# Optimization experiments

Measured on AMD Instinct MI355X. Metric: run time of the kernel, lower is better.

Reference implementation:

```python
import jax, jax.numpy as jnp
import numpy as np

B = 1048576
EPS = 1e-5

def _lin_params(key, din, dout):
    k1, k2 = jax.random.split(key)
    bound = 1.0 / np.sqrt(din)
    w = jax.random.uniform(k1, (din, dout), minval=-bound, maxval=bound, dtype=jnp.float32)
    b = jax.random.uniform(k2, (dout,), minval=-bound, maxval=bound, dtype=jnp.float32)
    return w, b

def setup_inputs() -> dict:
    key = jax.random.key(0)
    ks = jax.random.split(key, 10)
    x = jax.random.normal(ks[0], (B, 8), dtype=jnp.float32)
    dims = [(8, 16), (16, 16), (16, 12), (12, 8), (8, 4), (4, 4), (4, 4), (4, 1)]
    names = ['fm', 'c1', 'p1', 'c2', 'p2', 'c3', 'r', 'h']
    inp = {'x': x,
           'bn_g': jnp.ones((8,), jnp.float32),
           'bn_b': jnp.zeros((8,), jnp.float32)}
    for i, (nm, (di, do)) in enumerate(zip(names, dims)):
        w, b = _lin_params(ks[i + 1], di, do)
        inp['w_' + nm] = w
        inp['b_' + nm] = b
    return inp

def reference(x, bn_g, bn_b, w_fm, b_fm, w_c1, b_c1, w_p1, b_p1, w_c2, b_c2,
              w_p2, b_p2, w_c3, b_c3, w_r, b_r, w_h, b_h):
    # BatchNorm1d (training mode): batch statistics, biased variance
    mu = jnp.mean(x, axis=0)
    var = jnp.mean((x - mu) ** 2, axis=0)
    h = (x - mu) * jax.lax.rsqrt(var + EPS) * bn_g + bn_b
    h = jnp.tanh(h @ w_fm + b_fm)   # [B,16] feature_map
    h = jnp.tanh(h @ w_c1 + b_c1)   # [B,16] conv1
    h = jnp.tanh(h @ w_p1 + b_p1)   # [B,12] pool1
    h = jnp.tanh(h @ w_c2 + b_c2)   # [B,8]  conv2
    h = jnp.tanh(h @ w_p2 + b_p2)   # [B,4]  pool2
    h = jnp.tanh(h @ w_c3 + b_c3)   # [B,4]  conv3
    res = jax.nn.relu(h @ w_r + b_r)  # [B,4] residual branch
    h = h + res
    return jax.nn.sigmoid(h @ w_h + b_h)  # [B,1]
```

## Files before the change

kernel.cpp:

```cpp
#include <hip/hip_runtime.h>
#include <stdint.h>

#define B_ROWS 1048576
#define STAT_BLOCKS 512
#define MAIN_BLOCKS 2048

typedef __fp16 h2 __attribute__((ext_vector_type(2)));

#define PART_OFF 16
#define WPK_OFF 8208
#define BIA_OFF 8578
#define W_FM 0
#define W_C1 64
#define W_P1 192
#define W_C2 288
#define W_P2 336
#define W_C3 352
#define W_R  360
#define W_H  368
#define B_FM 0
#define B_C1 16
#define B_P1 32
#define B_C2 44
#define B_P2 52
#define B_C3 56
#define B_R  60
#define B_H  64

__device__ __forceinline__ float exp_tanh(float x) {
    float e = __builtin_amdgcn_exp2f(x * 2.8853900817779268f);
    return 1.0f - 2.0f * __builtin_amdgcn_rcpf(e + 1.0f);
}

__device__ __forceinline__ float fast_sigmoid(float x) {
    float e = __builtin_amdgcn_exp2f(x * -1.4426950408889634f);
    return __builtin_amdgcn_rcpf(1.0f + e);
}

template<int DIN, int DOUT>
__device__ void pack_layer(const float* __restrict__ w, const float* __restrict__ b,
                           uint32_t* __restrict__ wdst, float* __restrict__ bdst) {
    for (int idx = threadIdx.x; idx < DOUT * (DIN / 2); idx += blockDim.x) {
        int j = idx / (DIN / 2), i2 = idx % (DIN / 2);
        h2 h;
        h.x = (__fp16)w[(2 * i2) * DOUT + j];
        h.y = (__fp16)w[(2 * i2 + 1) * DOUT + j];
        wdst[j * (DIN / 2) + i2] = __builtin_bit_cast(uint32_t, h);
    }
    for (int j = threadIdx.x; j < DOUT; j += blockDim.x) bdst[j] = b[j];
}

__global__ __launch_bounds__(256) void bn_stats(
    const float* __restrict__ x, float* __restrict__ ws,
    const float* __restrict__ w_c1, const float* __restrict__ b_c1,
    const float* __restrict__ w_p1, const float* __restrict__ b_p1,
    const float* __restrict__ w_c2, const float* __restrict__ b_c2,
    const float* __restrict__ w_p2, const float* __restrict__ b_p2,
    const float* __restrict__ w_c3, const float* __restrict__ b_c3,
    const float* __restrict__ w_r,  const float* __restrict__ b_r,
    const float* __restrict__ w_h,  const float* __restrict__ b_h)
{
    const int tid = blockIdx.x * 256 + threadIdx.x;
    float s[8], q[8];
#pragma unroll
    for (int c = 0; c < 8; ++c) { s[c] = 0.f; q[c] = 0.f; }
    const float4* x4 = (const float4*)x;
#pragma unroll
    for (int k = 0; k < 8; ++k) {
        int r = tid + k * 131072;
        float4 a = x4[2 * r];
        float4 b = x4[2 * r + 1];
        s[0] += a.x; s[1] += a.y; s[2] += a.z; s[3] += a.w;
        s[4] += b.x; s[5] += b.y; s[6] += b.z; s[7] += b.w;
        q[0] += a.x * a.x; q[1] += a.y * a.y; q[2] += a.z * a.z; q[3] += a.w * a.w;
        q[4] += b.x * b.x; q[5] += b.y * b.y; q[6] += b.z * b.z; q[7] += b.w * b.w;
    }
#pragma unroll
    for (int off = 32; off > 0; off >>= 1) {
#pragma unroll
        for (int c = 0; c < 8; ++c) {
            s[c] += __shfl_down(s[c], off);
            q[c] += __shfl_down(q[c], off);
        }
    }
    __shared__ float red[4][16];
    const int lane = threadIdx.x & 63;
    const int wave = threadIdx.x >> 6;
    if (lane == 0) {
#pragma unroll
        for (int c = 0; c < 8; ++c) { red[wave][c] = s[c]; red[wave][8 + c] = q[c]; }
    }
    __syncthreads();
    if (threadIdx.x < 16) {
        float acc = red[0][threadIdx.x] + red[1][threadIdx.x] +
                    red[2][threadIdx.x] + red[3][threadIdx.x];
        ws[PART_OFF + blockIdx.x * 16 + threadIdx.x] = acc;
    }
    if (blockIdx.x == 0) {
        uint32_t* wpk = (uint32_t*)(ws + WPK_OFF);
        float*    bpk = ws + BIA_OFF;
        pack_layer<16,16>(w_c1, b_c1, wpk + W_C1, bpk + B_C1);
        pack_layer<16,12>(w_p1, b_p1, wpk + W_P1, bpk + B_P1);
        pack_layer<12, 8>(w_c2, b_c2, wpk + W_C2, bpk + B_C2);
        pack_layer<8,  4>(w_p2, b_p2, wpk + W_P2, bpk + B_P2);
        pack_layer<4,  4>(w_c3, b_c3, wpk + W_C3, bpk + B_C3);
        pack_layer<4,  4>(w_r,  b_r,  wpk + W_R,  bpk + B_R);
        pack_layer<4,  1>(w_h,  b_h,  wpk + W_H,  bpk + B_H);
    }
}

__global__ __launch_bounds__(256) void bn_finalize(
    const float* __restrict__ bn_g, const float* __restrict__ bn_b,
    const float* __restrict__ w_fm, const float* __restrict__ b_fm,
    float* __restrict__ ws)
{
    __shared__ float accs[16][17];
    __shared__ float scs[8], shs[8];
    const int f = threadIdx.x & 15;
    const int chunk = threadIdx.x >> 4;
    const float* p = ws + PART_OFF + (chunk * 32) * 16 + f;
    float a = 0.f;
#pragma unroll 8
    for (int b = 0; b < 32; ++b) a += p[b * 16];
    accs[chunk][f] = a;
    __syncthreads();
    if (threadIdx.x < 16) {
        float t = 0.f;
#pragma unroll
        for (int c = 0; c < 16; ++c) t += accs[c][threadIdx.x];
        accs[0][threadIdx.x] = t;
    }
    __syncthreads();
    if (threadIdx.x < 8) {
        const float invB = 1.0f / (float)B_ROWS;
        int c = threadIdx.x;
        float mu  = accs[0][c] * invB;
        float var = fmaf(-mu, mu, accs[0][8 + c] * invB);
        float sv  = bn_g[c] * rsqrtf(var + 1e-5f);
        scs[c] = sv;
        shs[c] = fmaf(-mu, sv, bn_b[c]);
    }
    __syncthreads();
    if (threadIdx.x < 64) {
        int j = threadIdx.x >> 2, i2 = threadIdx.x & 3;
        h2 h;
        h.x = (__fp16)(w_fm[(2 * i2) * 16 + j]     * scs[2 * i2]);
        h.y = (__fp16)(w_fm[(2 * i2 + 1) * 16 + j] * scs[2 * i2 + 1]);
        ((uint32_t*)(ws + WPK_OFF))[W_FM + j * 4 + i2] = __builtin_bit_cast(uint32_t, h);
    }
    if (threadIdx.x < 16) {
        int j = threadIdx.x;
        float acc = b_fm[j];
#pragma unroll
        for (int i = 0; i < 8; ++i) acc = fmaf(shs[i], w_fm[i * 16 + j], acc);
        (ws + BIA_OFF)[B_FM + j] = acc;
    }
}

template<int DIN, int DOUT>
__device__ __forceinline__ void layer_dot1(const h2* __restrict__ apk,
                                           float* __restrict__ o,
                                           const uint32_t* __restrict__ wpk,
                                           const float* __restrict__ bias) {
#pragma unroll
    for (int j = 0; j < DOUT; ++j) {
        float acc = bias[j];
#pragma unroll
        for (int i2 = 0; i2 < DIN / 2; ++i2) {
            h2 w = __builtin_bit_cast(h2, wpk[j * (DIN / 2) + i2]);
            acc = __builtin_amdgcn_fdot2(apk[i2], w, acc, false);
        }
        o[j] = acc;
    }
}

template<int N>
__device__ __forceinline__ void tanh_pack1(const float* __restrict__ in,
                                           h2* __restrict__ pk) {
#pragma unroll
    for (int k = 0; k < N / 2; ++k) {
        float t0 = exp_tanh(in[2 * k]);
        float t1 = exp_tanh(in[2 * k + 1]);
        pk[k] = __builtin_amdgcn_cvt_pkrtz(t0, t1);
    }
}

__device__ __forceinline__ float row_forward(float4 x0, float4 x1,
        const uint32_t* __restrict__ wpk, const float* __restrict__ bpk) {
    h2 a[4];
    a[0] = __builtin_amdgcn_cvt_pkrtz(x0.x, x0.y);
    a[1] = __builtin_amdgcn_cvt_pkrtz(x0.z, x0.w);
    a[2] = __builtin_amdgcn_cvt_pkrtz(x1.x, x1.y);
    a[3] = __builtin_amdgcn_cvt_pkrtz(x1.z, x1.w);

    float o1[16]; h2 p1[8];
    layer_dot1<8, 16>(a, o1, wpk + W_FM, bpk + B_FM);
    tanh_pack1<16>(o1, p1);
    float o2[16]; h2 p2[8];
    layer_dot1<16,16>(p1, o2, wpk + W_C1, bpk + B_C1);
    tanh_pack1<16>(o2, p2);
    float o3[12]; h2 p3[6];
    layer_dot1<16,12>(p2, o3, wpk + W_P1, bpk + B_P1);
    tanh_pack1<12>(o3, p3);
    float o4[8]; h2 p4[4];
    layer_dot1<12, 8>(p3, o4, wpk + W_C2, bpk + B_C2);
    tanh_pack1<8>(o4, p4);
    float o5[4]; h2 p5[2];
    layer_dot1<8,  4>(p4, o5, wpk + W_P2, bpk + B_P2);
    tanh_pack1<4>(o5, p5);
    float c4[4];
    layer_dot1<4,  4>(p5, c4, wpk + W_C3, bpk + B_C3);

    float f[4];
#pragma unroll
    for (int j = 0; j < 4; ++j) f[j] = exp_tanh(c4[j]);
    h2 pc[2];
    pc[0] = __builtin_amdgcn_cvt_pkrtz(f[0], f[1]);
    pc[1] = __builtin_amdgcn_cvt_pkrtz(f[2], f[3]);
    float r4[4];
    layer_dot1<4,  4>(pc, r4, wpk + W_R, bpk + B_R);
#pragma unroll
    for (int j = 0; j < 4; ++j) f[j] += fmaxf(r4[j], 0.f);
    h2 ph[2];
    ph[0] = __builtin_amdgcn_cvt_pkrtz(f[0], f[1]);
    ph[1] = __builtin_amdgcn_cvt_pkrtz(f[2], f[3]);
    float oh[1];
    layer_dot1<4,  1>(ph, oh, wpk + W_H, bpk + B_H);
    return fast_sigmoid(oh[0]);
}

__global__ __launch_bounds__(256, 6) void qcnn_main(
    const float* __restrict__ x, const float* __restrict__ ws,
    float* __restrict__ out)
{
    const int tid = blockIdx.x * 256 + threadIdx.x;
    const int r0 = tid, r1 = tid + (B_ROWS / 2);
    const float4* x4 = (const float4*)x;
    float4 xa0 = x4[2 * r0], xa1 = x4[2 * r0 + 1];
    float4 xb0 = x4[2 * r1], xb1 = x4[2 * r1 + 1];

    const uint32_t* wpk = (const uint32_t*)(ws + WPK_OFF);
    const float*    bpk = ws + BIA_OFF;

    out[r0] = row_forward(xa0, xa1, wpk, bpk);
    out[r1] = row_forward(xb0, xb1, wpk, bpk);
}

extern "C" void kernel_launch(void* const* d_in, const int* in_sizes, int n_in,
                              void* d_out, int out_size, void* d_ws, size_t ws_size,
                              hipStream_t stream) {
    const float* x    = (const float*)d_in[0];
    const float* bn_g = (const float*)d_in[1];
    const float* bn_b = (const float*)d_in[2];
    const float* w_fm = (const float*)d_in[3];
    const float* b_fm = (const float*)d_in[4];
    const float* w_c1 = (const float*)d_in[5];
    const float* b_c1 = (const float*)d_in[6];
    const float* w_p1 = (const float*)d_in[7];
    const float* b_p1 = (const float*)d_in[8];
    const float* w_c2 = (const float*)d_in[9];
    const float* b_c2 = (const float*)d_in[10];
    const float* w_p2 = (const float*)d_in[11];
    const float* b_p2 = (const float*)d_in[12];
    const float* w_c3 = (const float*)d_in[13];
    const float* b_c3 = (const float*)d_in[14];
    const float* w_r  = (const float*)d_in[15];
    const float* b_r  = (const float*)d_in[16];
    const float* w_h  = (const float*)d_in[17];
    const float* b_h  = (const float*)d_in[18];
    float* out = (float*)d_out;
    float* ws  = (float*)d_ws;

    bn_stats<<<STAT_BLOCKS, 256, 0, stream>>>(
        x, ws, w_c1, b_c1, w_p1, b_p1, w_c2, b_c2,
        w_p2, b_p2, w_c3, b_c3, w_r, b_r, w_h, b_h);
    bn_finalize<<<1, 256, 0, stream>>>(bn_g, bn_b, w_fm, b_fm, ws);
    qcnn_main<<<MAIN_BLOCKS, 256, 0, stream>>>(x, ws, out);
}
```

Baseline: 139.2 us.

## Fold BN finalize into main kernel and process four rows per thread

Removes the single-block bn_finalize launch. Each main-kernel block now redundantly reduces the 512 partial sums to BN scale and shift, and applies them per row with FMAs before fp16 packing, instead of folding them into the first-layer weights. The main grid is halved so each thread handles four rows as two adjacent pairs with float2 output stores. This trades one kernel launch and its serialization for redundant per-block reduction work, extra per-row normalization arithmetic, and block-level synchronization at kernel start.

```diff
diff --git a/kernel.cpp b/kernel.cpp
--- a/kernel.cpp
+++ b/kernel.cpp
@@ -3,7 +3,7 @@
 
 #define B_ROWS 1048576
 #define STAT_BLOCKS 512
-#define MAIN_BLOCKS 2048
+#define MAIN_BLOCKS 1024
 
 typedef __fp16 h2 __attribute__((ext_vector_type(2)));
 
@@ -52,6 +52,7 @@
 
 __global__ __launch_bounds__(256) void bn_stats(
     const float* __restrict__ x, float* __restrict__ ws,
+    const float* __restrict__ w_fm, const float* __restrict__ b_fm,
     const float* __restrict__ w_c1, const float* __restrict__ b_c1,
     const float* __restrict__ w_p1, const float* __restrict__ b_p1,
     const float* __restrict__ w_c2, const float* __restrict__ b_c2,
@@ -99,6 +100,7 @@
     if (blockIdx.x == 0) {
         uint32_t* wpk = (uint32_t*)(ws + WPK_OFF);
         float*    bpk = ws + BIA_OFF;
+        pack_layer<8, 16>(w_fm, b_fm, wpk + W_FM, bpk + B_FM);
         pack_layer<16,16>(w_c1, b_c1, wpk + W_C1, bpk + B_C1);
         pack_layer<16,12>(w_p1, b_p1, wpk + W_P1, bpk + B_P1);
         pack_layer<12, 8>(w_c2, b_c2, wpk + W_C2, bpk + B_C2);
@@ -109,54 +111,6 @@
     }
 }
 
-__global__ __launch_bounds__(256) void bn_finalize(
-    const float* __restrict__ bn_g, const float* __restrict__ bn_b,
-    const float* __restrict__ w_fm, const float* __restrict__ b_fm,
-    float* __restrict__ ws)
-{
-    __shared__ float accs[16][17];
-    __shared__ float scs[8], shs[8];
-    const int f = threadIdx.x & 15;
-    const int chunk = threadIdx.x >> 4;
-    const float* p = ws + PART_OFF + (chunk * 32) * 16 + f;
-    float a = 0.f;
-#pragma unroll 8
-    for (int b = 0; b < 32; ++b) a += p[b * 16];
-    accs[chunk][f] = a;
-    __syncthreads();
-    if (threadIdx.x < 16) {
-        float t = 0.f;
-#pragma unroll
-        for (int c = 0; c < 16; ++c) t += accs[c][threadIdx.x];
-        accs[0][threadIdx.x] = t;
-    }
-    __syncthreads();
-    if (threadIdx.x < 8) {
-        const float invB = 1.0f / (float)B_ROWS;
-        int c = threadIdx.x;
-        float mu  = accs[0][c] * invB;
-        float var = fmaf(-mu, mu, accs[0][8 + c] * invB);
-        float sv  = bn_g[c] * rsqrtf(var + 1e-5f);
-        scs[c] = sv;
-        shs[c] = fmaf(-mu, sv, bn_b[c]);
-    }
-    __syncthreads();
-    if (threadIdx.x < 64) {
-        int j = threadIdx.x >> 2, i2 = threadIdx.x & 3;
-        h2 h;
-        h.x = (__fp16)(w_fm[(2 * i2) * 16 + j]     * scs[2 * i2]);
-        h.y = (__fp16)(w_fm[(2 * i2 + 1) * 16 + j] * scs[2 * i2 + 1]);
-        ((uint32_t*)(ws + WPK_OFF))[W_FM + j * 4 + i2] = __builtin_bit_cast(uint32_t, h);
-    }
-    if (threadIdx.x < 16) {
-        int j = threadIdx.x;
-        float acc = b_fm[j];
-#pragma unroll
-        for (int i = 0; i < 8; ++i) acc = fmaf(shs[i], w_fm[i * 16 + j], acc);
-        (ws + BIA_OFF)[B_FM + j] = acc;
-    }
-}
-
 template<int DIN, int DOUT>
 __device__ __forceinline__ void layer_dot1(const h2* __restrict__ apk,
                                            float* __restrict__ o,
@@ -186,12 +140,17 @@
 }
 
 __device__ __forceinline__ float row_forward(float4 x0, float4 x1,
+        const float* __restrict__ sc, const float* __restrict__ sh,
         const uint32_t* __restrict__ wpk, const float* __restrict__ bpk) {
+    float n[8];
+    n[0] = fmaf(x0.x, sc[0], sh[0]); n[1] = fmaf(x0.y, sc[1], sh[1]);
+    n[2] = fmaf(x0.z, sc[2], sh[2]); n[3] = fmaf(x0.w, sc[3], sh[3]);
+    n[4] = fmaf(x1.x, sc[4], sh[4]); n[5] = fmaf(x1.y, sc[5], sh[5]);
+    n[6] = fmaf(x1.z, sc[6], sh[6]); n[7] = fmaf(x1.w, sc[7], sh[7]);
     h2 a[4];
-    a[0] = __builtin_amdgcn_cvt_pkrtz(x0.x, x0.y);
-    a[1] = __builtin_amdgcn_cvt_pkrtz(x0.z, x0.w);
-    a[2] = __builtin_amdgcn_cvt_pkrtz(x1.x, x1.y);
-    a[3] = __builtin_amdgcn_cvt_pkrtz(x1.z, x1.w);
+#pragma unroll
+    for (int k = 0; k < 4; ++k)
+        a[k] = __builtin_amdgcn_cvt_pkrtz(n[2 * k], n[2 * k + 1]);
 
     float o1[16]; h2 p1[8];
     layer_dot1<8, 16>(a, o1, wpk + W_FM, bpk + B_FM);
@@ -230,20 +189,68 @@
 }
 
 __global__ __launch_bounds__(256, 6) void qcnn_main(
-    const float* __restrict__ x, const float* __restrict__ ws,
-    float* __restrict__ out)
+    const float* __restrict__ x,
+    const float* __restrict__ bn_g, const float* __restrict__ bn_b,
+    const float* __restrict__ ws, float* __restrict__ out)
 {
     const int tid = blockIdx.x * 256 + threadIdx.x;
-    const int r0 = tid, r1 = tid + (B_ROWS / 2);
     const float4* x4 = (const float4*)x;
-    float4 xa0 = x4[2 * r0], xa1 = x4[2 * r0 + 1];
-    float4 xb0 = x4[2 * r1], xb1 = x4[2 * r1 + 1];
+    float4 xa0 = x4[4 * tid],     xa1 = x4[4 * tid + 1];
+    float4 xb0 = x4[4 * tid + 2], xb1 = x4[4 * tid + 3];
+
+    __shared__ float accs[16][17];
+    __shared__ float scs[8], shs[8];
+
+    {
+        const int f = threadIdx.x & 15;
+        const int chunk = threadIdx.x >> 4;
+        const float* p = ws + PART_OFF + (chunk * 32) * 16 + f;
+        float a = 0.f;
+#pragma unroll 8
+        for (int b = 0; b < 32; ++b) a += p[b * 16];
+        accs[chunk][f] = a;
+    }
+    __syncthreads();
+    if (threadIdx.x < 16) {
+        float t = 0.f;
+#pragma unroll
+        for (int c = 0; c < 16; ++c) t += accs[c][threadIdx.x];
+        accs[0][threadIdx.x] = t;
+    }
+    __syncthreads();
+    if (threadIdx.x < 8) {
+        const float invB = 1.0f / (float)B_ROWS;
+        int c = threadIdx.x;
+        float mu  = accs[0][c] * invB;
+        float var = fmaf(-mu, mu, accs[0][8 + c] * invB);
+        float sv  = bn_g[c] * rsqrtf(var + 1e-5f);
+        scs[c] = sv;
+        shs[c] = fmaf(-mu, sv, bn_b[c]);
+    }
+    __syncthreads();
+
+    float sc[8], sh[8];
+#pragma unroll
+    for (int c = 0; c < 8; ++c) { sc[c] = scs[c]; sh[c] = shs[c]; }
 
     const uint32_t* wpk = (const uint32_t*)(ws + WPK_OFF);
     const float*    bpk = ws + BIA_OFF;
 
-    out[r0] = row_forward(xa0, xa1, wpk, bpk);
-    out[r1] = row_forward(xb0, xb1, wpk, bpk);
+    {
+        float2 o2;
+        o2.x = row_forward(xa0, xa1, sc, sh, wpk, bpk);
+        o2.y = row_forward(xb0, xb1, sc, sh, wpk, bpk);
+        ((float2*)out)[tid] = o2;
+    }
+    {
+        const int t2 = tid + MAIN_BLOCKS * 256;
+        float4 ya0 = x4[4 * t2],     ya1 = x4[4 * t2 + 1];
+        float4 yb0 = x4[4 * t2 + 2], yb1 = x4[4 * t2 + 3];
+        float2 o2;
+        o2.x = row_forward(ya0, ya1, sc, sh, wpk, bpk);
+        o2.y = row_forward(yb0, yb1, sc, sh, wpk, bpk);
+        ((float2*)out)[t2] = o2;
+    }
 }
 
 extern "C" void kernel_launch(void* const* d_in, const int* in_sizes, int n_in,
@@ -272,8 +279,7 @@
     float* ws  = (float*)d_ws;
 
     bn_stats<<<STAT_BLOCKS, 256, 0, stream>>>(
-        x, ws, w_c1, b_c1, w_p1, b_p1, w_c2, b_c2,
+        x, ws, w_fm, b_fm, w_c1, b_c1, w_p1, b_p1, w_c2, b_c2,
         w_p2, b_p2, w_c3, b_c3, w_r, b_r, w_h, b_h);
-    bn_finalize<<<1, 256, 0, stream>>>(bn_g, bn_b, w_fm, b_fm, ws);
-    qcnn_main<<<MAIN_BLOCKS, 256, 0, stream>>>(x, ws, out);
-}
+    qcnn_main<<<MAIN_BLOCKS, 256, 0, stream>>>(x, bn_g, bn_b, ws, out);
+}
```

Result: slower. 157.9 us (+13.4%).
